# Kernel optimization log

Hardware: AMD Instinct MI355X
Metric: run time of the kernel (lower is better)

## Reference

```python
import jax, jax.numpy as jnp
import numpy as np

WINDOW_SIZE = 11
SIGMA = 1.5
C1 = 0.01 ** 2
C2 = 0.03 ** 2
L1_WEIGHT = 1.0
SSIM_WEIGHT = 1.0


def _gaussian_window(channels, window_size=WINDOW_SIZE, sigma=SIGMA):
    x = np.arange(window_size, dtype=np.float32) - window_size // 2
    g = np.exp(-(x ** 2) / (2.0 * sigma ** 2))
    g = g / g.sum()
    w2d = np.outer(g, g).astype(np.float32)  # [ws, ws]
    # depthwise kernel layout OIHW with I=1, O=channels
    return jnp.asarray(np.tile(w2d[None, None], (channels, 1, 1, 1)))


def _dwconv(x, w):
    pad = WINDOW_SIZE // 2
    return jax.lax.conv_general_dilated(
        x, w, window_strides=(1, 1), padding=[(pad, pad), (pad, pad)],
        dimension_numbers=('NCHW', 'OIHW', 'NCHW'),
        feature_group_count=x.shape[1])


def setup_inputs() -> dict:
    key = jax.random.key(0)
    k1, k2 = jax.random.split(key)
    shape = (16, 3, 512, 512)
    outputs = jax.random.uniform(k1, shape, dtype=jnp.float32)
    labels = jax.random.uniform(k2, shape, dtype=jnp.float32)
    return {"outputs": outputs, "labels": labels}


def reference(outputs, labels):
    img1, img2 = outputs, labels
    channel = img1.shape[1]
    window = _gaussian_window(channel).astype(img1.dtype)

    mu1 = _dwconv(img1, window)
    mu2 = _dwconv(img2, window)
    mu1_sq = mu1 * mu1
    mu2_sq = mu2 * mu2
    mu1_mu2 = mu1 * mu2
    sigma1_sq = _dwconv(img1 * img1, window) - mu1_sq
    sigma2_sq = _dwconv(img2 * img2, window) - mu2_sq
    sigma12 = _dwconv(img1 * img2, window) - mu1_mu2

    ssim_map = ((2 * mu1_mu2 + C1) * (2 * sigma12 + C2)) / (
        (mu1_sq + mu2_sq + C1) * (sigma1_sq + sigma2_sq + C2))
    ssim = jnp.mean(ssim_map)

    l1_loss = jnp.mean(jnp.abs(outputs - labels))
    ssim_loss = 1.0 - ssim
    return L1_WEIGHT * l1_loss + SSIM_WEIGHT * ssim_loss
```

## Files before the change

kernel.cpp:

```cpp
#include <hip/hip_runtime.h>
#include <hip/hip_bf16.h>
#include <math.h>

#define IMG 512
#define TS 32
#define NT 16
#define NIMG 48
#define NBLOCKS (NT * NT * NIMG)
#define NPIX (16LL * 3 * 512 * 512)

#define C1F 0.0001f
#define C2F 0.0009f

#define SROW 56
#define SROWS 48
#define TCOLS 32

typedef __attribute__((ext_vector_type(8))) short short8;
typedef __attribute__((ext_vector_type(4))) float float4v;

#define GW0 0.00102838f
#define GW1 0.00759877f
#define GW2 0.03600077f
#define GW3 0.10936069f
#define GW4 0.21300539f
#define GW5 0.26601172f

__device__ __forceinline__ unsigned short f2bf(float f) {
    unsigned u = __builtin_bit_cast(unsigned, f);
    u += 0x7FFF + ((u >> 16) & 1);
    return (unsigned short)(u >> 16);
}
__device__ __forceinline__ unsigned pk2(float a, float b) {
    __hip_bfloat162 h = __float22bfloat162_rn(make_float2(a, b));
    unsigned u;
    __builtin_memcpy(&u, &h, 4);
    return u;
}

__global__ __launch_bounds__(256, 5)
void ssim_tile_kernel(const float* __restrict__ xg, const float* __restrict__ yg,
                      float* __restrict__ partials) {
    __shared__ unsigned short sbuf[2][SROWS][SROW];
    __shared__ unsigned short tbuf[5][TCOLS][SROW];
    __shared__ unsigned short gwtbl[16];
    __shared__ float red[8];

    const int tid  = threadIdx.x;
    const int lane = tid & 63;
    const int w    = tid >> 6;
    const int q    = lane >> 4;
    const int n16  = lane & 15;

    const int img = blockIdx.z;
    const int r00  = blockIdx.y * TS - 5;
    const int c00a = blockIdx.x * TS - 8;
    const float* __restrict__ xi = xg + (size_t)img * (IMG * IMG);
    const float* __restrict__ yi = yg + (size_t)img * (IMG * IMG);

    if (tid < 16) {
        const float gwf[11] = {GW0, GW1, GW2, GW3, GW4, GW5, GW4, GW3, GW2, GW1, GW0};
        unsigned short v = 0;
        #pragma unroll
        for (int t = 0; t < 11; ++t)
            if (tid == t) v = f2bf(gwf[t]);
        gwtbl[tid] = v;
    }

    for (int u = tid; u < 576; u += 256) {
        int pr  = u / 12;
        int pc4 = (u - pr * 12) << 2;
        int gr = r00 + pr, gc = c00a + pc4;
        float4 xv = make_float4(0.f, 0.f, 0.f, 0.f);
        float4 yv = make_float4(0.f, 0.f, 0.f, 0.f);
        if (pr < 42 && (unsigned)gr < 512u && (unsigned)gc < 512u) {
            size_t o = (size_t)gr * IMG + gc;
            xv = *(const float4*)(xi + o);
            yv = *(const float4*)(yi + o);
        }
        *(uint2*)&sbuf[0][pr][pc4] = make_uint2(pk2(xv.x, xv.y), pk2(xv.z, xv.w));
        *(uint2*)&sbuf[1][pr][pc4] = make_uint2(pk2(yv.x, yv.y), pk2(yv.z, yv.w));
    }

    float l1_loc;
    {
        int r  = tid >> 3;
        int c4 = (tid & 7) << 2;
        size_t o = (size_t)(blockIdx.y * TS + r) * IMG + blockIdx.x * TS + c4;
        float4 a = *(const float4*)(xi + o);
        float4 b = *(const float4*)(yi + o);
        l1_loc = fabsf(a.x - b.x) + fabsf(a.y - b.y) + fabsf(a.z - b.z) + fabsf(a.w - b.w);
    }
    __syncthreads();

    short8 bh, bv;
    {
        int baseh = q * 8 - n16 - 3;
        int basev = q * 8 - n16;
        #pragma unroll
        for (int j = 0; j < 8; ++j) {
            unsigned ih = min((unsigned)(baseh + j), 15u);
            unsigned iv = min((unsigned)(basev + j), 15u);
            bh[j] = (short)gwtbl[ih];
            bv[j] = (short)gwtbl[iv];
        }
    }

    for (int u = w; u < 6; u += 4) {
        int rg = u >> 1, cg = u & 1;
        short8 ax = *(const short8*)&sbuf[0][rg * 16 + n16][cg * 16 + q * 8];
        short8 ay = *(const short8*)&sbuf[1][rg * 16 + n16][cg * 16 + q * 8];
        short8 axx, ayy, axy;
        {
            unsigned* px = (unsigned*)&ax;
            unsigned* py = (unsigned*)&ay;
            unsigned* pxx = (unsigned*)&axx;
            unsigned* pyy = (unsigned*)&ayy;
            unsigned* pxy = (unsigned*)&axy;
            #pragma unroll
            for (int r = 0; r < 4; ++r) {
                unsigned rx = px[r], ry = py[r];
                float xlo = __builtin_bit_cast(float, rx << 16);
                float xhi = __builtin_bit_cast(float, rx & 0xFFFF0000u);
                float ylo = __builtin_bit_cast(float, ry << 16);
                float yhi = __builtin_bit_cast(float, ry & 0xFFFF0000u);
                pxx[r] = pk2(xlo * xlo, xhi * xhi);
                pyy[r] = pk2(ylo * ylo, yhi * yhi);
                pxy[r] = pk2(xlo * ylo, xhi * yhi);
            }
        }
        float4v d;
        d = __builtin_amdgcn_mfma_f32_16x16x32_bf16(ax, bh, (float4v){0.f,0.f,0.f,0.f}, 0, 0, 0);
        *(uint2*)&tbuf[0][cg * 16 + n16][rg * 16 + q * 4] = make_uint2(pk2(d[0], d[1]), pk2(d[2], d[3]));
        d = __builtin_amdgcn_mfma_f32_16x16x32_bf16(ay, bh, (float4v){0.f,0.f,0.f,0.f}, 0, 0, 0);
        *(uint2*)&tbuf[1][cg * 16 + n16][rg * 16 + q * 4] = make_uint2(pk2(d[0], d[1]), pk2(d[2], d[3]));
        d = __builtin_amdgcn_mfma_f32_16x16x32_bf16(axx, bh, (float4v){0.f,0.f,0.f,0.f}, 0, 0, 0);
        *(uint2*)&tbuf[2][cg * 16 + n16][rg * 16 + q * 4] = make_uint2(pk2(d[0], d[1]), pk2(d[2], d[3]));
        d = __builtin_amdgcn_mfma_f32_16x16x32_bf16(ayy, bh, (float4v){0.f,0.f,0.f,0.f}, 0, 0, 0);
        *(uint2*)&tbuf[3][cg * 16 + n16][rg * 16 + q * 4] = make_uint2(pk2(d[0], d[1]), pk2(d[2], d[3]));
        d = __builtin_amdgcn_mfma_f32_16x16x32_bf16(axy, bh, (float4v){0.f,0.f,0.f,0.f}, 0, 0, 0);
        *(uint2*)&tbuf[4][cg * 16 + n16][rg * 16 + q * 4] = make_uint2(pk2(d[0], d[1]), pk2(d[2], d[3]));
    }
    __syncthreads();

    const int rgp = w >> 1, cgp = w & 1;
    float4v acc5[5];
    #pragma unroll
    for (int ch = 0; ch < 5; ++ch) {
        short8 a = *(const short8*)&tbuf[ch][cgp * 16 + n16][rgp * 16 + q * 8];
        acc5[ch] = __builtin_amdgcn_mfma_f32_16x16x32_bf16(
            a, bv, (float4v){0.f, 0.f, 0.f, 0.f}, 0, 0, 0);
    }

    float ssim_loc = 0.f;
    #pragma unroll
    for (int r = 0; r < 4; ++r) {
        float mu1 = acc5[0][r], mu2 = acc5[1][r];
        float e11 = acc5[2][r], e22 = acc5[3][r], e12 = acc5[4][r];
        float m1s = mu1 * mu1, m2s = mu2 * mu2, m12 = mu1 * mu2;
        float v1 = e11 - m1s, v2 = e22 - m2s, v12 = e12 - m12;
        float num = (2.f * m12 + C1F) * (2.f * v12 + C2F);
        float den = (m1s + m2s + C1F) * (v1 + v2 + C2F);
        ssim_loc = fmaf(num, __builtin_amdgcn_rcpf(den), ssim_loc);
    }

    #pragma unroll
    for (int off = 32; off > 0; off >>= 1) {
        ssim_loc += __shfl_down(ssim_loc, off);
        l1_loc   += __shfl_down(l1_loc, off);
    }
    if (lane == 0) {
        red[w] = ssim_loc;
        red[4 + w] = l1_loc;
    }
    __syncthreads();
    if (tid == 0) {
        float ss = red[0] + red[1] + red[2] + red[3];
        float ll = red[4] + red[5] + red[6] + red[7];
        int bid = blockIdx.x + NT * (blockIdx.y + NT * blockIdx.z);
        partials[bid] = ss;
        partials[NBLOCKS + bid] = ll;
    }
}

__global__ __launch_bounds__(1024)
void finalize_kernel(const float* __restrict__ partials, float* __restrict__ out) {
    __shared__ double rs[16], rl[16];
    const int tid = threadIdx.x;
    double ss = 0.0, ll = 0.0;
    for (int i = tid; i < NBLOCKS; i += 1024) {
        ss += (double)partials[i];
        ll += (double)partials[NBLOCKS + i];
    }
    #pragma unroll
    for (int off = 32; off > 0; off >>= 1) {
        ss += __shfl_down(ss, off);
        ll += __shfl_down(ll, off);
    }
    int wave = tid >> 6, lane = tid & 63;
    if (lane == 0) { rs[wave] = ss; rl[wave] = ll; }
    __syncthreads();
    if (tid == 0) {
        double sst = 0.0, llt = 0.0;
        #pragma unroll
        for (int w = 0; w < 16; ++w) { sst += rs[w]; llt += rl[w]; }
        double invn = 1.0 / (double)NPIX;
        out[0] = (float)(llt * invn + (1.0 - sst * invn));
    }
}

extern "C" void kernel_launch(void* const* d_in, const int* in_sizes, int n_in,
                              void* d_out, int out_size, void* d_ws, size_t ws_size,
                              hipStream_t stream) {
    const float* x = (const float*)d_in[0];
    const float* y = (const float*)d_in[1];
    float* out = (float*)d_out;
    float* partials = (float*)d_ws;

    dim3 grid(NT, NT, NIMG);
    ssim_tile_kernel<<<grid, dim3(256), 0, stream>>>(x, y, partials);
    finalize_kernel<<<1, dim3(1024), 0, stream>>>(partials, out);
}
```

Before: 154.0 us.

## Widen SSIM tiles to 64x32 to cut halo overhead per output

```diff
diff --git a/kernel.cpp b/kernel.cpp
--- a/kernel.cpp
+++ b/kernel.cpp
@@ -3,18 +3,19 @@
 #include <math.h>
 
 #define IMG 512
-#define TS 32
-#define NT 16
+#define TW 64
+#define TH 32
+#define NTX 8
+#define NTY 16
 #define NIMG 48
-#define NBLOCKS (NT * NT * NIMG)
+#define NBLOCKS (NTX * NTY * NIMG)
 #define NPIX (16LL * 3 * 512 * 512)
 
 #define C1F 0.0001f
 #define C2F 0.0009f
 
-#define SROW 56
-#define SROWS 48
-#define TCOLS 32
+#define SR 88
+#define TR 56
 
 typedef __attribute__((ext_vector_type(8))) short short8;
 typedef __attribute__((ext_vector_type(4))) float float4v;
@@ -38,11 +39,11 @@
     return u;
 }
 
-__global__ __launch_bounds__(256, 5)
+__global__ __launch_bounds__(256, 3)
 void ssim_tile_kernel(const float* __restrict__ xg, const float* __restrict__ yg,
                       float* __restrict__ partials) {
-    __shared__ unsigned short sbuf[2][SROWS][SROW];
-    __shared__ unsigned short tbuf[5][TCOLS][SROW];
+    __shared__ unsigned short sbuf[2][48][SR];
+    __shared__ unsigned short tbuf[5][TW][TR];
     __shared__ unsigned short gwtbl[16];
     __shared__ float red[8];
 
@@ -53,8 +54,8 @@
     const int n16  = lane & 15;
 
     const int img = blockIdx.z;
-    const int r00  = blockIdx.y * TS - 5;
-    const int c00a = blockIdx.x * TS - 8;
+    const int r00  = blockIdx.y * TH - 5;
+    const int c00a = blockIdx.x * TW - 8;
     const float* __restrict__ xi = xg + (size_t)img * (IMG * IMG);
     const float* __restrict__ yi = yg + (size_t)img * (IMG * IMG);
 
@@ -67,9 +68,9 @@
         gwtbl[tid] = v;
     }
 
-    for (int u = tid; u < 576; u += 256) {
-        int pr  = u / 12;
-        int pc4 = (u - pr * 12) << 2;
+    for (int u = tid; u < 960; u += 256) {
+        int pr  = u / 20;
+        int pc4 = (u - pr * 20) << 2;
         int gr = r00 + pr, gc = c00a + pc4;
         float4 xv = make_float4(0.f, 0.f, 0.f, 0.f);
         float4 yv = make_float4(0.f, 0.f, 0.f, 0.f);
@@ -85,11 +86,14 @@
     float l1_loc;
     {
         int r  = tid >> 3;
-        int c4 = (tid & 7) << 2;
-        size_t o = (size_t)(blockIdx.y * TS + r) * IMG + blockIdx.x * TS + c4;
-        float4 a = *(const float4*)(xi + o);
-        float4 b = *(const float4*)(yi + o);
-        l1_loc = fabsf(a.x - b.x) + fabsf(a.y - b.y) + fabsf(a.z - b.z) + fabsf(a.w - b.w);
+        int c8 = (tid & 7) << 3;
+        size_t o = (size_t)(blockIdx.y * TH + r) * IMG + blockIdx.x * TW + c8;
+        float4 a0 = *(const float4*)(xi + o);
+        float4 a1 = *(const float4*)(xi + o + 4);
+        float4 b0 = *(const float4*)(yi + o);
+        float4 b1 = *(const float4*)(yi + o + 4);
+        l1_loc = fabsf(a0.x - b0.x) + fabsf(a0.y - b0.y) + fabsf(a0.z - b0.z) + fabsf(a0.w - b0.w)
+               + fabsf(a1.x - b1.x) + fabsf(a1.y - b1.y) + fabsf(a1.z - b1.z) + fabsf(a1.w - b1.w);
     }
     __syncthreads();
 
@@ -106,8 +110,10 @@
         }
     }
 
-    for (int u = w; u < 6; u += 4) {
-        int rg = u >> 1, cg = u & 1;
+    #pragma unroll
+    for (int i = 0; i < 3; ++i) {
+        int u = w + i * 4;
+        int rg = u >> 2, cg = u & 3;
         short8 ax = *(const short8*)&sbuf[0][rg * 16 + n16][cg * 16 + q * 8];
         short8 ay = *(const short8*)&sbuf[1][rg * 16 + n16][cg * 16 + q * 8];
         short8 axx, ayy, axy;
@@ -143,25 +149,26 @@
     }
     __syncthreads();
 
-    const int rgp = w >> 1, cgp = w & 1;
-    float4v acc5[5];
-    #pragma unroll
-    for (int ch = 0; ch < 5; ++ch) {
-        short8 a = *(const short8*)&tbuf[ch][cgp * 16 + n16][rgp * 16 + q * 8];
-        acc5[ch] = __builtin_amdgcn_mfma_f32_16x16x32_bf16(
-            a, bv, (float4v){0.f, 0.f, 0.f, 0.f}, 0, 0, 0);
-    }
-
     float ssim_loc = 0.f;
     #pragma unroll
-    for (int r = 0; r < 4; ++r) {
-        float mu1 = acc5[0][r], mu2 = acc5[1][r];
-        float e11 = acc5[2][r], e22 = acc5[3][r], e12 = acc5[4][r];
-        float m1s = mu1 * mu1, m2s = mu2 * mu2, m12 = mu1 * mu2;
-        float v1 = e11 - m1s, v2 = e22 - m2s, v12 = e12 - m12;
-        float num = (2.f * m12 + C1F) * (2.f * v12 + C2F);
-        float den = (m1s + m2s + C1F) * (v1 + v2 + C2F);
-        ssim_loc = fmaf(num, __builtin_amdgcn_rcpf(den), ssim_loc);
+    for (int rgp = 0; rgp < 2; ++rgp) {
+        float4v acc5[5];
+        #pragma unroll
+        for (int ch = 0; ch < 5; ++ch) {
+            short8 a = *(const short8*)&tbuf[ch][w * 16 + n16][rgp * 16 + q * 8];
+            acc5[ch] = __builtin_amdgcn_mfma_f32_16x16x32_bf16(
+                a, bv, (float4v){0.f, 0.f, 0.f, 0.f}, 0, 0, 0);
+        }
+        #pragma unroll
+        for (int r = 0; r < 4; ++r) {
+            float mu1 = acc5[0][r], mu2 = acc5[1][r];
+            float e11 = acc5[2][r], e22 = acc5[3][r], e12 = acc5[4][r];
+            float m1s = mu1 * mu1, m2s = mu2 * mu2, m12 = mu1 * mu2;
+            float v1 = e11 - m1s, v2 = e22 - m2s, v12 = e12 - m12;
+            float num = (2.f * m12 + C1F) * (2.f * v12 + C2F);
+            float den = (m1s + m2s + C1F) * (v1 + v2 + C2F);
+            ssim_loc = fmaf(num, __builtin_amdgcn_rcpf(den), ssim_loc);
+        }
     }
 
     #pragma unroll
@@ -177,7 +184,7 @@
     if (tid == 0) {
         float ss = red[0] + red[1] + red[2] + red[3];
         float ll = red[4] + red[5] + red[6] + red[7];
-        int bid = blockIdx.x + NT * (blockIdx.y + NT * blockIdx.z);
+        int bid = blockIdx.x + NTX * (blockIdx.y + NTY * blockIdx.z);
         partials[bid] = ss;
         partials[NBLOCKS + bid] = ll;
     }
@@ -217,7 +224,7 @@
     float* out = (float*)d_out;
     float* partials = (float*)d_ws;
 
-    dim3 grid(NT, NT, NIMG);
+    dim3 grid(NTX, NTY, NIMG);
     ssim_tile_kernel<<<grid, dim3(256), 0, stream>>>(x, y, partials);
     finalize_kernel<<<1, dim3(1024), 0, stream>>>(partials, out);
 }
```

Result: slower. 157.3 us (+2.1%).
